# Kernel optimization log

Hardware: AMD Instinct MI355X
Metric: run time of the kernel (lower is better)

Reference implementation:

```python
import jax, jax.numpy as jnp
from jax import lax
import numpy as np

KEY = 4
WIDTH = 32
CH = 3


def _inv_perm():
    # Reproduce construct_mapping(4, 32, 3): mapping[0] = arange(384),
    # mapping[1] = blocks of a (4,32,3) index grid split into 4x4x3 column
    # blocks, flattened. tensor_map does out[:, perm] = in[:, arange], i.e.
    # a scatter; equivalently out = in[:, argsort(perm)].
    s = np.arange(KEY * WIDTH * CH).reshape(KEY, WIDTH, CH)
    perm = np.concatenate([s[:, j:j + KEY, :].reshape(-1) for j in range(0, WIDTH, KEY)])
    return np.argsort(perm)  # (384,)

_INV = jnp.asarray(_inv_perm())


def _conv(x, w, b):
    y = lax.conv_general_dilated(x, w, (1, 1), 'SAME',
                                 dimension_numbers=('NCHW', 'OIHW', 'NCHW'))
    return y + b[None, :, None, None]


def _maxpool2(x):
    return lax.reduce_window(x, -jnp.inf, lax.max,
                             (1, 1, 2, 2), (1, 1, 2, 2), 'VALID')


def setup_inputs() -> dict:
    key = jax.random.key(0)
    ks = jax.random.split(key, 10)
    f32 = jnp.float32
    B = 8192
    return {
        'x': jax.random.normal(ks[0], (B, 32, 32, 3), dtype=f32),
        'W_lin': jax.random.normal(ks[1], (48, 48), dtype=f32) * 0.1,
        'conv1_w': jax.random.normal(ks[2], (32, 3, 3, 3), dtype=f32) * 0.1,
        'conv1_b': jax.random.normal(ks[3], (32,), dtype=f32) * 0.05,
        'conv2_w': jax.random.normal(ks[4], (64, 32, 3, 3), dtype=f32) * 0.05,
        'conv2_b': jax.random.normal(ks[5], (64,), dtype=f32) * 0.05,
        'conv3_w': jax.random.normal(ks[6], (128, 64, 3, 3), dtype=f32) * 0.05,
        'conv3_b': jax.random.normal(ks[7], (128,), dtype=f32) * 0.05,
        'fc_w': jax.random.normal(ks[8], (10, 2048), dtype=f32) * 0.02,
        'fc_b': jax.random.normal(ks[9], (10,), dtype=f32) * 0.02,
        'stage': 2,
    }


def reference(x, W_lin, conv1_w, conv1_b, conv2_w, conv2_b, conv3_w, conv3_b,
              fc_w, fc_b, stage):
    B = x.shape[0]
    if stage == 2:
        # 64 blocks of 4x4x3 in row-major block order (i outer, j inner).
        xb = x.reshape(B, 8, KEY, 8, KEY, CH)            # (B, ib, ir, jb, jc, c)
        xb = xb.transpose(0, 1, 3, 2, 4, 5).reshape(B, 64, 48)
        y = jnp.einsum('bnk,ok->bno', xb, W_lin)          # per-block linear (no bias)
        # group 8 column-blocks per row-block -> (B, 8, 384), permute columns
        y = y.reshape(B, 8, 384)[:, :, _INV]
        x_final = y.reshape(B, 32, 32, 3).transpose(0, 3, 1, 2)  # NCHW
    else:
        x_final = x
    h = _maxpool2(jax.nn.relu(_conv(x_final, conv1_w, conv1_b)))
    h = _maxpool2(jax.nn.relu(_conv(h, conv2_w, conv2_b)))
    h = _maxpool2(jax.nn.relu(_conv(h, conv3_w, conv3_b)))
    h = h.reshape(-1, 2048)
    logits = h @ fc_w.T + fc_b
    return jax.nn.log_softmax(logits, axis=-1)
```

## Files before the change

### kernel.cpp

```cpp
#include <hip/hip_runtime.h>
#include <hip/hip_bf16.h>

typedef unsigned short u16;
typedef __attribute__((ext_vector_type(8))) short short8v;
typedef __attribute__((ext_vector_type(4))) float f32x4;
typedef __attribute__((ext_vector_type(16))) float f32x16;
typedef union { short8v v; uint u[4]; } pack8;

__device__ __forceinline__ float bu2f(u16 u) {
    return __uint_as_float(((unsigned)u) << 16);
}
__device__ __forceinline__ u16 f2bu(float f) {
    unsigned u = __float_as_uint(f);
    u += 0x7fffu + ((u >> 16) & 1u);
    return (u16)(u >> 16);
}
__device__ __forceinline__ uint pk2(float a, float b) {
    return (uint)f2bu(a) | ((uint)f2bu(b) << 16);
}

__global__ __launch_bounds__(256) void k_repack(
    const float* __restrict__ Wlin, const float* __restrict__ c1w,
    const float* __restrict__ c2w, const float* __restrict__ c3w,
    u16* __restrict__ w1p, u16* __restrict__ s2wp,
    u16* __restrict__ w2p, u16* __restrict__ w3p)
{
    int i = blockIdx.x * 256 + threadIdx.x;
    if (i < 32 * 72) {
        int oc = i / 72, k = i - oc * 72;
        int kh = k >> 4, e = k & 15;
        u16 v = 0;
        if (kh < 3 && e < 9) {
            int kw = e / 3, c = e - kw * 3;
            v = f2bu(c1w[((oc * 3 + c) * 3 + kh) * 3 + kw]);
        }
        w1p[i] = v;
    }
    if (i < 96 * 72) {
        int r = i / 72, k = i - r * 72;
        u16 v = 0;
        if (k < 48) {
            int o = r % 48;
            float w = Wlin[o * 48 + k];
            u16 hi = f2bu(w);
            v = (r < 48) ? hi : f2bu(w - bu2f(hi));
        }
        s2wp[i] = v;
    }
    if (i < 64 * 288) {
        int oc = i / 288, r = i - oc * 288;
        int tap = r >> 5, ic = r & 31;
        w2p[oc * 296 + r] = f2bu(c2w[(oc * 32 + ic) * 9 + tap]);
    }
    if (i < 128 * 576) {
        int oc = i / 576, r = i - oc * 576;
        int tap = r >> 6, ic = r & 63;
        w3p[oc * 584 + r] = f2bu(c3w[(oc * 64 + ic) * 9 + tap]);
    }
}

#define IMG_E 0
#define IMG_O 3488
#define XB    6976
#define S2W   11584
#define IN3   6976
#define W1L   18496
#define IN2   20800
#define LDS_N 33760

__global__ __launch_bounds__(256) void k_img(
    const float* __restrict__ x, const u16* __restrict__ s2wp,
    const u16* __restrict__ w1p, const float* __restrict__ c1b,
    const int* __restrict__ stage,
    const u16* __restrict__ w2p, const float* __restrict__ c2b,
    const u16* __restrict__ w3p, const float* __restrict__ c3b,
    u16* __restrict__ o3)
{
    __shared__ __align__(16) u16 lds[LDS_N];
    const int b = blockIdx.x, t = threadIdx.x;
    const int wv = t >> 6, lane = t & 63, lr = lane & 15, q = lane >> 4;
    uint* z32 = (uint*)lds;

    for (int i = t; i < 3488; i += 256) z32[i] = 0u;
    for (int i = t; i < 1360; i += 256) {
        int cell = i / 20, d = i - cell * 20;
        int h, w;
        if (cell < 18)      { h = 0;  w = cell; }
        else if (cell < 36) { h = 17; w = cell - 18; }
        else { int k = cell - 36; h = 1 + (k >> 1); w = (k & 1) * 17; }
        z32[10400 + (h * 18 + w) * 20 + d] = 0u;
    }
    for (int i = t; i < 864; i += 256)
        *(short8v*)(&lds[S2W + i * 8]) = *(const short8v*)(&s2wp[i * 8]);
    for (int i = t; i < 288; i += 256)
        *(short8v*)(&lds[W1L + i * 8]) = *(const short8v*)(&w1p[i * 8]);

    const int sv = stage[0];
    if (sv == 2) {
        {
            const int n = t >> 2, ir = t & 3;
            const float* xp = x + (size_t)b * 3072 + (((n >> 3) * 4 + ir) * 96 + (n & 7) * 12);
            const float4 va = ((const float4*)xp)[0];
            const float4 vb = ((const float4*)xp)[1];
            const float4 vc = ((const float4*)xp)[2];
            uint* dst = (uint*)&lds[XB + n * 72 + ir * 12];
            dst[0] = pk2(va.x, va.y); dst[1] = pk2(va.z, va.w);
            dst[2] = pk2(vb.x, vb.y); dst[3] = pk2(vb.z, vb.w);
            dst[4] = pk2(vc.x, vc.y); dst[5] = pk2(vc.z, vc.w);
            if (ir < 2) {
                uint* z2 = (uint*)&lds[XB + n * 72 + 48 + ir * 8];
                z2[0] = 0u; z2[1] = 0u; z2[2] = 0u; z2[3] = 0u;
            }
        }
        __syncthreads();
        short8v a0 = *(const short8v*)&lds[XB + (wv * 16 + lr) * 72 + q * 8];
        short8v a1 = *(const short8v*)&lds[XB + (wv * 16 + lr) * 72 + 32 + q * 8];
        f32x4 y[3];
        #pragma unroll
        for (int nf = 0; nf < 3; ++nf) {
            y[nf] = (f32x4){0.f, 0.f, 0.f, 0.f};
            short8v bh0 = *(const short8v*)&lds[S2W + (nf * 16 + lr) * 72 + q * 8];
            short8v bh1 = *(const short8v*)&lds[S2W + (nf * 16 + lr) * 72 + 32 + q * 8];
            short8v bl0 = *(const short8v*)&lds[S2W + (48 + nf * 16 + lr) * 72 + q * 8];
            short8v bl1 = *(const short8v*)&lds[S2W + (48 + nf * 16 + lr) * 72 + 32 + q * 8];
            y[nf] = __builtin_amdgcn_mfma_f32_16x16x32_bf16(a0, bh0, y[nf], 0, 0, 0);
            y[nf] = __builtin_amdgcn_mfma_f32_16x16x32_bf16(a1, bh1, y[nf], 0, 0, 0);
            y[nf] = __builtin_amdgcn_mfma_f32_16x16x32_bf16(a0, bl0, y[nf], 0, 0, 0);
            y[nf] = __builtin_amdgcn_mfma_f32_16x16x32_bf16(a1, bl1, y[nf], 0, 0, 0);
        }
        __syncthreads();
        #pragma unroll
        for (int nf = 0; nf < 3; ++nf)
            #pragma unroll
            for (int r = 0; r < 4; ++r) {
                int n2 = wv * 16 + q * 4 + r;
                int o  = nf * 16 + lr;
                int ir = o / 12, rm = o - ir * 12;
                int jc = rm / 3, c = rm - jc * 3;
                int hh = (n2 >> 3) * 4 + ir, ww = (n2 & 7) * 4 + jc;
                int e  = ((hh + 1) * 34 + (ww + 1)) * 3 + c;
                u16 val = f2bu(y[nf][r]);
                lds[IMG_E + e] = val;
                lds[IMG_O + e - 1] = val;
            }
    } else {
        __syncthreads();
        for (int e = t; e < 3072; e += 256) {
            int hh = e / 96, rm = e - hh * 96;
            int ww = rm / 3, c = rm - ww * 3;
            u16 val = f2bu(x[(size_t)b * 3072 + e]);
            int ii = ((hh + 1) * 34 + (ww + 1)) * 3 + c;
            lds[IMG_E + ii] = val;
            lds[IMG_O + ii - 1] = val;
        }
    }
    __syncthreads();

    for (int i = t; i < 1152; i += 256) {
        int cell = i >> 5, d = i & 31;
        int pos;
        if (cell < 10)      pos = cell;
        else if (cell < 20) pos = 90 + (cell - 10);
        else { int k = cell - 20; pos = (1 + (k >> 1)) * 10 + (k & 1) * 9; }
        z32[3488 + pos * 32 + d] = 0u;
    }
    {
        const int oc32 = lane & 31, hi = lane >> 5;
        short8v wb[3];
        #pragma unroll
        for (int s = 0; s < 3; ++s)
            wb[s] = *(const short8v*)&lds[W1L + oc32 * 72 + s * 16 + hi * 8];
        const float bias1 = c1b[oc32];

        #pragma unroll
        for (int chk = 0; chk < 4; ++chk) {
            f32x16 acc0, acc1;
            #pragma unroll
            for (int i = 0; i < 16; ++i) { acc0[i] = 0.f; acc1[i] = 0.f; }
            #pragma unroll
            for (int s = 0; s < 3; ++s) {
                #pragma unroll
                for (int f = 0; f < 2; ++f) {
                    const int h = wv * 8 + chk * 2 + f;
                    const int a = 3 * ((h + s) * 34 + oc32) + hi * 8;
                    const uint* sp = (a & 1) ? (const uint*)&lds[IMG_O + a - 1]
                                             : (const uint*)&lds[IMG_E + a];
                    pack8 pk;
                    pk.u[0] = sp[0]; pk.u[1] = sp[1]; pk.u[2] = sp[2]; pk.u[3] = sp[3];
                    if (f == 0) acc0 = __builtin_amdgcn_mfma_f32_32x32x16_bf16(pk.v, wb[s], acc0, 0, 0, 0);
                    else        acc1 = __builtin_amdgcn_mfma_f32_32x32x16_bf16(pk.v, wb[s], acc1, 0, 0, 0);
                }
            }
            const int hq = wv * 4 + chk;
            #pragma unroll
            for (int g = 0; g < 4; ++g) {
                #pragma unroll
                for (int pp = 0; pp < 2; ++pp) {
                    float v = fmaxf(acc0[4 * g + 2 * pp] + bias1, 0.f);
                    v = fmaxf(v, fmaxf(acc0[4 * g + 2 * pp + 1] + bias1, 0.f));
                    v = fmaxf(v, fmaxf(acc1[4 * g + 2 * pp] + bias1, 0.f));
                    v = fmaxf(v, fmaxf(acc1[4 * g + 2 * pp + 1] + bias1, 0.f));
                    const int wq = 4 * g + 2 * hi + pp;
                    lds[IN2 + ((hq + 1) * 18 + (wq + 1)) * 40 + oc32] = f2bu(v);
                }
            }
        }
    }
    __syncthreads();

    {
        const u16* wb2 = w2p + (size_t)lr * 296 + q * 8;
        f32x4 acc[4][4];
        #pragma unroll
        for (int m = 0; m < 4; ++m)
            #pragma unroll
            for (int n = 0; n < 4; ++n) acc[m][n] = (f32x4){0.f, 0.f, 0.f, 0.f};

        short8v bfr[3][4];
        #pragma unroll
        for (int n = 0; n < 4; ++n) {
            bfr[0][n] = *(const short8v*)(wb2 + n * 4736 + 0);
            bfr[1][n] = *(const short8v*)(wb2 + n * 4736 + 32);
        }
        #pragma unroll
        for (int s = 0; s < 9; ++s) {
            if (s + 2 < 9) {
                #pragma unroll
                for (int n = 0; n < 4; ++n)
                    bfr[(s + 2) % 3][n] = *(const short8v*)(wb2 + n * 4736 + (s + 2) * 32);
            }
            const int kh = s / 3, kw = s - kh * 3;
            short8v af[4];
            #pragma unroll
            for (int m = 0; m < 4; ++m)
                af[m] = *(const short8v*)(&lds[IN2 + ((wv * 4 + m + kh) * 18 + lr + kw) * 40 + q * 8]);
            __builtin_amdgcn_s_setprio(1);
            #pragma unroll
            for (int m = 0; m < 4; ++m)
                #pragma unroll
                for (int n = 0; n < 4; ++n)
                    acc[m][n] = __builtin_amdgcn_mfma_f32_16x16x32_bf16(af[m], bfr[s % 3][n], acc[m][n], 0, 0, 0);
            __builtin_amdgcn_s_setprio(0);
        }
        #pragma unroll
        for (int n = 0; n < 4; ++n) {
            float bias = c2b[n * 16 + lr];
            #pragma unroll
            for (int mp = 0; mp < 2; ++mp) {
                #pragma unroll
                for (int p = 0; p < 2; ++p) {
                    float v = fmaxf(acc[2 * mp][n][2 * p] + bias, 0.f);
                    v = fmaxf(v, fmaxf(acc[2 * mp][n][2 * p + 1] + bias, 0.f));
                    v = fmaxf(v, fmaxf(acc[2 * mp + 1][n][2 * p] + bias, 0.f));
                    v = fmaxf(v, fmaxf(acc[2 * mp + 1][n][2 * p + 1] + bias, 0.f));
                    int hq = wv * 2 + mp, wq = 2 * q + p;
                    int posW = (hq + 1) * 10 + (wq + 1);
                    int oc = n * 16 + lr;
                    lds[IN3 + posW * 64 + (oc ^ ((posW & 7) << 3))] = f2bu(v);
                }
            }
        }
    }
    __syncthreads();

    {
        const int ocb = wv * 32;
        const int hA = lr >> 3, wA = lr & 7;
        const u16* wb3 = w3p + (size_t)(ocb + lr) * 584 + q * 8;

        f32x4 acc3[4][2];
        #pragma unroll
        for (int m = 0; m < 4; ++m)
            #pragma unroll
            for (int n = 0; n < 2; ++n) acc3[m][n] = (f32x4){0.f, 0.f, 0.f, 0.f};

        short8v br[3][2];
        #pragma unroll
        for (int n = 0; n < 2; ++n) {
            br[0][n] = *(const short8v*)(wb3 + n * 9344 + 0);
            br[1][n] = *(const short8v*)(wb3 + n * 9344 + 32);
        }
        #pragma unroll
        for (int s = 0; s < 18; ++s) {
            if (s + 2 < 18) {
                const int off2 = ((s + 2) >> 1) * 64 + ((s + 2) & 1) * 32;
                #pragma unroll
                for (int n = 0; n < 2; ++n)
                    br[(s + 2) % 3][n] = *(const short8v*)(wb3 + n * 9344 + off2);
            }
            const int tap = s >> 1, half = s & 1;
            const int kh = tap / 3, kw = tap - kh * 3;
            short8v a3[4];
            #pragma unroll
            for (int m = 0; m < 4; ++m) {
                int posR = (m * 2 + hA + kh) * 10 + wA + kw;
                int sl = (half * 32 + q * 8) ^ ((posR & 7) << 3);
                a3[m] = *(const short8v*)(&lds[IN3 + posR * 64 + sl]);
            }
            __builtin_amdgcn_s_setprio(1);
            #pragma unroll
            for (int m = 0; m < 4; ++m)
                #pragma unroll
                for (int n = 0; n < 2; ++n)
                    acc3[m][n] = __builtin_amdgcn_mfma_f32_16x16x32_bf16(a3[m], br[s % 3][n], acc3[m][n], 0, 0, 0);
            __builtin_amdgcn_s_setprio(0);
        }
        #pragma unroll
        for (int n = 0; n < 2; ++n) {
            float bias = c3b[ocb + n * 16 + lr];
            #pragma unroll
            for (int m = 0; m < 4; ++m) {
                #pragma unroll
                for (int p = 0; p < 2; ++p) {
                    float v = fmaxf(acc3[m][n][2 * p] + bias, 0.f);
                    v = fmaxf(v, fmaxf(acc3[m][n][2 * p + 1] + bias, 0.f));
                    float v2 = fmaxf(v, __shfl_xor(v, 32));
                    if (lane < 32) {
                        int wq = (q & 1) * 2 + p;
                        o3[(size_t)b * 2048 + (m * 4 + wq) * 128 + ocb + n * 16 + lr] = f2bu(v2);
                    }
                }
            }
        }
    }
}

__global__ __launch_bounds__(256) void k_fc(
    const u16* __restrict__ o3, const float* __restrict__ fw,
    const float* __restrict__ fb, float* __restrict__ out)
{
    const int b = blockIdx.x * 4 + (threadIdx.x >> 6);
    const int lane = threadIdx.x & 63;
    const u16* xp = o3 + (size_t)b * 2048;
    float xr[32];
    #pragma unroll
    for (int i = 0; i < 32; ++i) {
        int kk = lane + i * 64;
        int c = kk >> 4, h = (kk >> 2) & 3, w = kk & 3;
        xr[i] = bu2f(xp[h * 512 + w * 128 + c]);
    }
    float lg[10];
    #pragma unroll
    for (int o = 0; o < 10; ++o) {
        const float* wr = fw + (size_t)o * 2048;
        float s = 0.f;
        #pragma unroll
        for (int i = 0; i < 32; ++i) s += xr[i] * wr[lane + i * 64];
        #pragma unroll
        for (int d = 32; d > 0; d >>= 1) s += __shfl_xor(s, d);
        lg[o] = s + fb[o];
    }
    float m = lg[0];
    #pragma unroll
    for (int o = 1; o < 10; ++o) m = fmaxf(m, lg[o]);
    float den = 0.f;
    #pragma unroll
    for (int o = 0; o < 10; ++o) den += expf(lg[o] - m);
    float lse = logf(den);
    if (lane < 10) {
        float v = lg[0];
        #pragma unroll
        for (int o = 1; o < 10; ++o) v = (lane == o) ? lg[o] : v;
        out[(size_t)b * 10 + lane] = v - m - lse;
    }
}

extern "C" void kernel_launch(void* const* d_in, const int* in_sizes, int n_in,
                              void* d_out, int out_size, void* d_ws, size_t ws_size,
                              hipStream_t stream)
{
    const float* x    = (const float*)d_in[0];
    const float* Wlin = (const float*)d_in[1];
    const float* c1w  = (const float*)d_in[2];
    const float* c1b  = (const float*)d_in[3];
    const float* c2w  = (const float*)d_in[4];
    const float* c2b  = (const float*)d_in[5];
    const float* c3w  = (const float*)d_in[6];
    const float* c3b  = (const float*)d_in[7];
    const float* fw   = (const float*)d_in[8];
    const float* fb   = (const float*)d_in[9];
    const int* stage  = (const int*)d_in[10];
    float* out = (float*)d_out;

    const int B = in_sizes[0] / 3072;

    char* ws = (char*)d_ws;
    u16* o3   = (u16*)ws;
    char* WB  = ws + (size_t)B * 4096;
    u16* w1p  = (u16*)(WB);
    u16* s2wp = (u16*)(WB + 4608);
    u16* w2p  = (u16*)(WB + 18432);
    u16* w3p  = (u16*)(WB + 56320);

    k_repack<<<288, 256, 0, stream>>>(Wlin, c1w, c2w, c3w, w1p, s2wp, w2p, w3p);
    k_img   <<<B, 256, 0, stream>>>(x, s2wp, w1p, c1b, stage, w2p, c2b, w3p, c3b, o3);
    k_fc    <<<B / 4, 256, 0, stream>>>(o3, fw, fb, out);
}
```

Before: 287.4 us.

## Pad conv1 input image to 4 channels and load linear weights into registers

The conv1 input image moves from two offset 3-channel copies (even and odd) to a single 4-channel padded layout. Each MFMA A fragment is now two aligned 64-bit LDS loads, and conv1 weights are repacked to match (K=48). The stage-2 linear weights are read straight from global memory into registers instead of being staged in LDS, which removes a barrier and shrinks LDS use, possibly allowing higher occupancy. The pool epilogues now take the max before adding bias and applying ReLU, which cuts per-element adds and maxes.

```diff
diff --git a/kernel.cpp b/kernel.cpp
--- a/kernel.cpp
+++ b/kernel.cpp
@@ -26,14 +26,13 @@
     u16* __restrict__ w2p, u16* __restrict__ w3p)
 {
     int i = blockIdx.x * 256 + threadIdx.x;
-    if (i < 32 * 72) {
-        int oc = i / 72, k = i - oc * 72;
+    if (i < 32 * 48) {
+        int oc = i / 48, k = i - oc * 48;
         int kh = k >> 4, e = k & 15;
+        int kw = e >> 2, c = e & 3;
         u16 v = 0;
-        if (kh < 3 && e < 9) {
-            int kw = e / 3, c = e - kw * 3;
+        if (kw < 3 && c < 3)
             v = f2bu(c1w[((oc * 3 + c) * 3 + kh) * 3 + kw]);
-        }
         w1p[i] = v;
     }
     if (i < 96 * 72) {
@@ -59,14 +58,12 @@
     }
 }
 
-#define IMG_E 0
-#define IMG_O 3488
-#define XB    6976
-#define S2W   11584
-#define IN3   6976
-#define W1L   18496
-#define IN2   20800
-#define LDS_N 33760
+#define IMG4  0
+#define SCR   4624
+#define IN3   4624
+#define W1L   11024
+#define IN2   12560
+#define LDS_N 25520
 
 __global__ __launch_bounds__(256) void k_img(
     const float* __restrict__ x, const u16* __restrict__ s2wp,
@@ -81,18 +78,16 @@
     const int wv = t >> 6, lane = t & 63, lr = lane & 15, q = lane >> 4;
     uint* z32 = (uint*)lds;
 
-    for (int i = t; i < 3488; i += 256) z32[i] = 0u;
+    for (int i = t; i < 2312; i += 256) z32[i] = 0u;
     for (int i = t; i < 1360; i += 256) {
         int cell = i / 20, d = i - cell * 20;
         int h, w;
         if (cell < 18)      { h = 0;  w = cell; }
         else if (cell < 36) { h = 17; w = cell - 18; }
         else { int k = cell - 36; h = 1 + (k >> 1); w = (k & 1) * 17; }
-        z32[10400 + (h * 18 + w) * 20 + d] = 0u;
-    }
-    for (int i = t; i < 864; i += 256)
-        *(short8v*)(&lds[S2W + i * 8]) = *(const short8v*)(&s2wp[i * 8]);
-    for (int i = t; i < 288; i += 256)
+        z32[6280 + (h * 18 + w) * 20 + d] = 0u;
+    }
+    for (int i = t; i < 192; i += 256)
         *(short8v*)(&lds[W1L + i * 8]) = *(const short8v*)(&w1p[i * 8]);
 
     const int sv = stage[0];
@@ -103,32 +98,35 @@
             const float4 va = ((const float4*)xp)[0];
             const float4 vb = ((const float4*)xp)[1];
             const float4 vc = ((const float4*)xp)[2];
-            uint* dst = (uint*)&lds[XB + n * 72 + ir * 12];
+            uint* dst = (uint*)&lds[SCR + n * 72 + ir * 12];
             dst[0] = pk2(va.x, va.y); dst[1] = pk2(va.z, va.w);
             dst[2] = pk2(vb.x, vb.y); dst[3] = pk2(vb.z, vb.w);
             dst[4] = pk2(vc.x, vc.y); dst[5] = pk2(vc.z, vc.w);
             if (ir < 2) {
-                uint* z2 = (uint*)&lds[XB + n * 72 + 48 + ir * 8];
+                uint* z2 = (uint*)&lds[SCR + n * 72 + 48 + ir * 8];
                 z2[0] = 0u; z2[1] = 0u; z2[2] = 0u; z2[3] = 0u;
             }
         }
+        short8v bh0[3], bh1[3], bl0[3], bl1[3];
+        #pragma unroll
+        for (int nf = 0; nf < 3; ++nf) {
+            bh0[nf] = *(const short8v*)(&s2wp[(nf * 16 + lr) * 72 + q * 8]);
+            bh1[nf] = *(const short8v*)(&s2wp[(nf * 16 + lr) * 72 + 32 + q * 8]);
+            bl0[nf] = *(const short8v*)(&s2wp[(48 + nf * 16 + lr) * 72 + q * 8]);
+            bl1[nf] = *(const short8v*)(&s2wp[(48 + nf * 16 + lr) * 72 + 32 + q * 8]);
+        }
         __syncthreads();
-        short8v a0 = *(const short8v*)&lds[XB + (wv * 16 + lr) * 72 + q * 8];
-        short8v a1 = *(const short8v*)&lds[XB + (wv * 16 + lr) * 72 + 32 + q * 8];
+        short8v a0 = *(const short8v*)&lds[SCR + (wv * 16 + lr) * 72 + q * 8];
+        short8v a1 = *(const short8v*)&lds[SCR + (wv * 16 + lr) * 72 + 32 + q * 8];
         f32x4 y[3];
         #pragma unroll
         for (int nf = 0; nf < 3; ++nf) {
             y[nf] = (f32x4){0.f, 0.f, 0.f, 0.f};
-            short8v bh0 = *(const short8v*)&lds[S2W + (nf * 16 + lr) * 72 + q * 8];
-            short8v bh1 = *(const short8v*)&lds[S2W + (nf * 16 + lr) * 72 + 32 + q * 8];
-            short8v bl0 = *(const short8v*)&lds[S2W + (48 + nf * 16 + lr) * 72 + q * 8];
-            short8v bl1 = *(const short8v*)&lds[S2W + (48 + nf * 16 + lr) * 72 + 32 + q * 8];
-            y[nf] = __builtin_amdgcn_mfma_f32_16x16x32_bf16(a0, bh0, y[nf], 0, 0, 0);
-            y[nf] = __builtin_amdgcn_mfma_f32_16x16x32_bf16(a1, bh1, y[nf], 0, 0, 0);
-            y[nf] = __builtin_amdgcn_mfma_f32_16x16x32_bf16(a0, bl0, y[nf], 0, 0, 0);
-            y[nf] = __builtin_amdgcn_mfma_f32_16x16x32_bf16(a1, bl1, y[nf], 0, 0, 0);
-        }
-        __syncthreads();
+            y[nf] = __builtin_amdgcn_mfma_f32_16x16x32_bf16(a0, bh0[nf], y[nf], 0, 0, 0);
+            y[nf] = __builtin_amdgcn_mfma_f32_16x16x32_bf16(a1, bh1[nf], y[nf], 0, 0, 0);
+            y[nf] = __builtin_amdgcn_mfma_f32_16x16x32_bf16(a0, bl0[nf], y[nf], 0, 0, 0);
+            y[nf] = __builtin_amdgcn_mfma_f32_16x16x32_bf16(a1, bl1[nf], y[nf], 0, 0, 0);
+        }
         #pragma unroll
         for (int nf = 0; nf < 3; ++nf)
             #pragma unroll
@@ -138,20 +136,15 @@
                 int ir = o / 12, rm = o - ir * 12;
                 int jc = rm / 3, c = rm - jc * 3;
                 int hh = (n2 >> 3) * 4 + ir, ww = (n2 & 7) * 4 + jc;
-                int e  = ((hh + 1) * 34 + (ww + 1)) * 3 + c;
-                u16 val = f2bu(y[nf][r]);
-                lds[IMG_E + e] = val;
-                lds[IMG_O + e - 1] = val;
+                lds[IMG4 + ((hh + 1) * 34 + (ww + 1)) * 4 + c] = f2bu(y[nf][r]);
             }
     } else {
+        if (t < 4) z32[2312 + t] = 0u;
         __syncthreads();
         for (int e = t; e < 3072; e += 256) {
             int hh = e / 96, rm = e - hh * 96;
             int ww = rm / 3, c = rm - ww * 3;
-            u16 val = f2bu(x[(size_t)b * 3072 + e]);
-            int ii = ((hh + 1) * 34 + (ww + 1)) * 3 + c;
-            lds[IMG_E + ii] = val;
-            lds[IMG_O + ii - 1] = val;
+            lds[IMG4 + ((hh + 1) * 34 + (ww + 1)) * 4 + c] = f2bu(x[(size_t)b * 3072 + e]);
         }
     }
     __syncthreads();
@@ -162,14 +155,14 @@
         if (cell < 10)      pos = cell;
         else if (cell < 20) pos = 90 + (cell - 10);
         else { int k = cell - 20; pos = (1 + (k >> 1)) * 10 + (k & 1) * 9; }
-        z32[3488 + pos * 32 + d] = 0u;
+        z32[2312 + pos * 32 + d] = 0u;
     }
     {
         const int oc32 = lane & 31, hi = lane >> 5;
         short8v wb[3];
         #pragma unroll
         for (int s = 0; s < 3; ++s)
-            wb[s] = *(const short8v*)&lds[W1L + oc32 * 72 + s * 16 + hi * 8];
+            wb[s] = *(const short8v*)&lds[W1L + oc32 * 48 + s * 16 + hi * 8];
         const float bias1 = c1b[oc32];
 
         #pragma unroll
@@ -182,11 +175,10 @@
                 #pragma unroll
                 for (int f = 0; f < 2; ++f) {
                     const int h = wv * 8 + chk * 2 + f;
-                    const int a = 3 * ((h + s) * 34 + oc32) + hi * 8;
-                    const uint* sp = (a & 1) ? (const uint*)&lds[IMG_O + a - 1]
-                                             : (const uint*)&lds[IMG_E + a];
+                    const int a4 = ((h + s) * 34 + oc32 + hi * 2) * 4;
                     pack8 pk;
-                    pk.u[0] = sp[0]; pk.u[1] = sp[1]; pk.u[2] = sp[2]; pk.u[3] = sp[3];
+                    *(unsigned long long*)&pk.u[0] = *(const unsigned long long*)(&lds[IMG4 + a4]);
+                    *(unsigned long long*)&pk.u[2] = *(const unsigned long long*)(&lds[IMG4 + a4 + 4]);
                     if (f == 0) acc0 = __builtin_amdgcn_mfma_f32_32x32x16_bf16(pk.v, wb[s], acc0, 0, 0, 0);
                     else        acc1 = __builtin_amdgcn_mfma_f32_32x32x16_bf16(pk.v, wb[s], acc1, 0, 0, 0);
                 }
@@ -196,10 +188,10 @@
             for (int g = 0; g < 4; ++g) {
                 #pragma unroll
                 for (int pp = 0; pp < 2; ++pp) {
-                    float v = fmaxf(acc0[4 * g + 2 * pp] + bias1, 0.f);
-                    v = fmaxf(v, fmaxf(acc0[4 * g + 2 * pp + 1] + bias1, 0.f));
-                    v = fmaxf(v, fmaxf(acc1[4 * g + 2 * pp] + bias1, 0.f));
-                    v = fmaxf(v, fmaxf(acc1[4 * g + 2 * pp + 1] + bias1, 0.f));
+                    const int i0 = 4 * g + 2 * pp;
+                    float m0 = fmaxf(acc0[i0], acc0[i0 + 1]);
+                    float m1 = fmaxf(acc1[i0], acc1[i0 + 1]);
+                    float v = fmaxf(fmaxf(m0, m1) + bias1, 0.f);
                     const int wq = 4 * g + 2 * hi + pp;
                     lds[IN2 + ((hq + 1) * 18 + (wq + 1)) * 40 + oc32] = f2bu(v);
                 }
@@ -249,10 +241,9 @@
             for (int mp = 0; mp < 2; ++mp) {
                 #pragma unroll
                 for (int p = 0; p < 2; ++p) {
-                    float v = fmaxf(acc[2 * mp][n][2 * p] + bias, 0.f);
-                    v = fmaxf(v, fmaxf(acc[2 * mp][n][2 * p + 1] + bias, 0.f));
-                    v = fmaxf(v, fmaxf(acc[2 * mp + 1][n][2 * p] + bias, 0.f));
-                    v = fmaxf(v, fmaxf(acc[2 * mp + 1][n][2 * p + 1] + bias, 0.f));
+                    float m0 = fmaxf(acc[2 * mp][n][2 * p], acc[2 * mp][n][2 * p + 1]);
+                    float m1 = fmaxf(acc[2 * mp + 1][n][2 * p], acc[2 * mp + 1][n][2 * p + 1]);
+                    float v = fmaxf(fmaxf(m0, m1) + bias, 0.f);
                     int hq = wv * 2 + mp, wq = 2 * q + p;
                     int posW = (hq + 1) * 10 + (wq + 1);
                     int oc = n * 16 + lr;
@@ -312,12 +303,12 @@
             for (int m = 0; m < 4; ++m) {
                 #pragma unroll
                 for (int p = 0; p < 2; ++p) {
-                    float v = fmaxf(acc3[m][n][2 * p] + bias, 0.f);
-                    v = fmaxf(v, fmaxf(acc3[m][n][2 * p + 1] + bias, 0.f));
-                    float v2 = fmaxf(v, __shfl_xor(v, 32));
+                    float mm = fmaxf(acc3[m][n][2 * p], acc3[m][n][2 * p + 1]);
+                    float v2 = fmaxf(mm, __shfl_xor(mm, 32));
+                    float v = fmaxf(v2 + bias, 0.f);
                     if (lane < 32) {
                         int wq = (q & 1) * 2 + p;
-                        o3[(size_t)b * 2048 + (m * 4 + wq) * 128 + ocb + n * 16 + lr] = f2bu(v2);
+                        o3[(size_t)b * 2048 + (m * 4 + wq) * 128 + ocb + n * 16 + lr] = f2bu(v);
                     }
                 }
             }
```

After: 292.0 us. Within noise of the previous version (+1.6%).
